# Kernel optimization log

Hardware: AMD Instinct MI355X
Metric: run time of the kernel (lower is better)

Reference implementation:

```python
import jax, jax.numpy as jnp
import numpy as np

LEFT, RIGHT = 64, 64  # left_size, right_size; hidden = LEFT*RIGHT = 4096


def _cayley(raw):
    """torch nn.utils.parametrizations.orthogonal(..., orthogonal_map='cayley',
    use_trivialization=False): A = triu(raw, 1); X = A - A^T (skew-symmetric);
    Q = (I - X/2)^{-1} (I + X/2)."""
    n = raw.shape[0]
    A = jnp.triu(raw, 1)
    X = A - A.T
    Id = jnp.eye(n, dtype=raw.dtype)
    return jnp.linalg.solve(Id - 0.5 * X, Id + 0.5 * X)


def setup_inputs() -> dict:
    key = jax.random.key(0)
    ks = jax.random.split(key, 8)
    B, S = 4, 2048
    H = LEFT * RIGHT
    inp = jax.random.normal(ks[0], (B, S, H), dtype=jnp.float32)
    raw_u_left = jax.random.normal(ks[1], (LEFT, LEFT), dtype=jnp.float32) * 0.02
    raw_v_left = jax.random.normal(ks[2], (LEFT, LEFT), dtype=jnp.float32) * 0.02
    raw_u_right = jax.random.normal(ks[3], (RIGHT, RIGHT), dtype=jnp.float32) * 0.02
    raw_v_right = jax.random.normal(ks[4], (RIGHT, RIGHT), dtype=jnp.float32) * 0.02
    diag_left = jnp.ones((LEFT,), dtype=jnp.float32)
    diag_right = jnp.ones((RIGHT,), dtype=jnp.float32)
    diag_scale = jnp.ones((H,), dtype=jnp.float32) + 0.01 * jax.random.normal(ks[5], (H,), dtype=jnp.float32)
    return {
        "inp": inp,
        "raw_u_left": raw_u_left,
        "raw_v_left": raw_v_left,
        "diag_left": diag_left,
        "raw_u_right": raw_u_right,
        "raw_v_right": raw_v_right,
        "diag_right": diag_right,
        "diag_scale": diag_scale,
        "inv_t": 0,
    }


def reference(inp, raw_u_left, raw_v_left, diag_left, raw_u_right, raw_v_right,
              diag_right, diag_scale, inv_t):
    # add_diag=True, use_diag=True path
    if inv_t:
        x = inp / diag_scale
        dl = 1.0 / diag_left
        dr = 1.0 / diag_right
    else:
        x = inp * diag_scale
        dl = diag_left
        dr = diag_right
    # Cayley-parametrized orthogonal factors
    Ul = _cayley(raw_u_left)
    Vl = _cayley(raw_v_left)
    Ur = _cayley(raw_u_right)
    Vr = _cayley(raw_v_right)
    # SVD-style reconstruction: M = U @ diag(d) @ V^T
    ML = (Ul * dl[None, :]) @ Vl.T  # [LEFT, LEFT]
    MR = (Ur * dr[None, :]) @ Vr.T  # [RIGHT, RIGHT]
    # Kronecker matmul: view last dim as [LEFT, RIGHT], out = ML^T @ X @ MR
    orig_shape = x.shape
    xb = x.reshape(-1, LEFT, RIGHT)  # [B*S, LEFT, RIGHT]
    out = jnp.einsum('bij,ik,jl->bkl', xb, ML, MR)
    return out.reshape(orig_shape)
```

## Files before the change

### kernel.cpp

```cpp
#include <hip/hip_runtime.h>
#include <hip/hip_bf16.h>

typedef short short8 __attribute__((ext_vector_type(8)));
typedef short short4v __attribute__((ext_vector_type(4)));
typedef float f32x4 __attribute__((ext_vector_type(4)));

#define HID 4096
#define CST 68

__device__ __forceinline__ unsigned short f2bf(float f) {
    unsigned int u = __float_as_uint(f);
    u = (u + 0x7FFFu + ((u >> 16) & 1u)) >> 16;
    return (unsigned short)u;
}

__device__ __forceinline__ f32x4 mm4(const float* SA, const float* SB, int i, int j0) {
    f32x4 acc = {0.f, 0.f, 0.f, 0.f};
#pragma unroll 8
    for (int k = 0; k < 64; ++k) {
        float a = SA[i * CST + k];
        acc += a * *reinterpret_cast<const f32x4*>(SB + k * CST + j0);
    }
    return acc;
}

__global__ __launch_bounds__(1024) void cayley_build_kernel(
    const float* __restrict__ rul, const float* __restrict__ rvl, const float* __restrict__ dl,
    const float* __restrict__ rur, const float* __restrict__ rvr, const float* __restrict__ dr,
    const int* __restrict__ invt,
    unsigned short* __restrict__ plb, unsigned short* __restrict__ mrtb)
{
    __shared__ __align__(16) float Yw[64 * CST], Aw[64 * CST], Pw[64 * CST];
    __shared__ __align__(16) float Qw[64 * CST], QTw[64 * CST];
    __shared__ float dd[64];

    const float* ru; const float* rv; const float* dv; unsigned short* ob;
    if (blockIdx.x == 0) { ru = rul; rv = rvl; dv = dl; ob = plb; }
    else                 { ru = rur; rv = rvr; dv = dr; ob = mrtb; }

    const int tid = threadIdx.x;
    const int i = tid >> 4;
    const int j0 = (tid & 15) << 2;

    for (int pass = 0; pass < 2; ++pass) {
        const float* raw = (pass == 0) ? ru : rv;
#pragma unroll
        for (int q = 0; q < 4; ++q) {
            int j = j0 + q;
            float v = 0.f;
            if (j > i)      v =  raw[i * 64 + j];
            else if (j < i) v = -raw[j * 64 + i];
            Yw[i * CST + j] = 0.5f * v;
        }
        __syncthreads();
        f32x4 a = mm4(Yw, Yw, i, j0);
        __syncthreads();
        *reinterpret_cast<f32x4*>(Aw + i * CST + j0) = a;
        *reinterpret_cast<f32x4*>(Pw + i * CST + j0) =
            a + *reinterpret_cast<const f32x4*>(Yw + i * CST + j0);
        __syncthreads();
        a = mm4(Pw, Aw, i, j0);
        __syncthreads();
        *reinterpret_cast<f32x4*>(Pw + i * CST + j0) += a;
        __syncthreads();
        a = mm4(Aw, Aw, i, j0);
        __syncthreads();
        *reinterpret_cast<f32x4*>(Aw + i * CST + j0) = a;
        __syncthreads();
        a = mm4(Pw, Aw, i, j0);
        __syncthreads();
        f32x4 p = *reinterpret_cast<const f32x4*>(Pw + i * CST + j0) + a;
#pragma unroll
        for (int q = 0; q < 4; ++q) {
            int j = j0 + q;
            float qv = ((i == j) ? 1.f : 0.f) + 2.f * p[q];
            if (pass == 0) Qw[i * CST + j]  = qv;
            else           QTw[j * CST + i] = qv;
        }
        __syncthreads();
    }
    if (tid < 64) { float d = dv[tid]; dd[tid] = (invt[0] != 0) ? (1.0f / d) : d; }
    __syncthreads();

    f32x4 m = {0.f, 0.f, 0.f, 0.f};
#pragma unroll 8
    for (int j = 0; j < 64; ++j) {
        float aa = Qw[i * CST + j] * dd[j];
        m += aa * *reinterpret_cast<const f32x4*>(QTw + j * CST + j0);
    }
#pragma unroll
    for (int q = 0; q < 4; ++q)
        ob[(j0 + q) * 64 + i] = f2bf(m[q]);
}

__global__ __launch_bounds__(256) void kron_kernel(
    const float* __restrict__ inp, const float* __restrict__ ds,
    const unsigned short* __restrict__ plb, const unsigned short* __restrict__ mrtb,
    const int* __restrict__ invt, float* __restrict__ out, int ntok)
{
    __shared__ __align__(16) unsigned short zbuf[4][64 * 72];
    const int w = threadIdx.x >> 6;
    const int lane = threadIdx.x & 63;
    const int l15 = lane & 15;
    const int lg = lane >> 4;
    unsigned short* Zt = zbuf[w];
    const int rowoff = l15 * 64 + lg * 8;

    short8 bmr[2][4], bpl[2][4];
#pragma unroll
    for (int tc = 0; tc < 4; ++tc)
#pragma unroll
        for (int s = 0; s < 2; ++s) {
            bmr[s][tc] = *reinterpret_cast<const short8*>(
                mrtb + (tc * 16 + l15) * 64 + s * 32 + lg * 8);
            bpl[s][tc] = *reinterpret_cast<const short8*>(
                plb + (tc * 16 + l15) * 64 + s * 32 + lg * 8);
        }
    const bool inv = (invt[0] != 0);

    const int t0 = (blockIdx.x * 4 + w) * 2;
#pragma unroll
    for (int it = 0; it < 2; ++it) {
        const int t = t0 + it;
        if (t >= ntok) break;
        const float* xt = inp + (size_t)t * HID;

        f32x4 acc[4][4];
        {
            f32x4 z = {0.f, 0.f, 0.f, 0.f};
#pragma unroll
            for (int a = 0; a < 4; ++a)
#pragma unroll
                for (int b = 0; b < 4; ++b) acc[a][b] = z;
        }
#pragma unroll
        for (int tr = 0; tr < 4; ++tr) {
            short8 a1[2];
#pragma unroll
            for (int s = 0; s < 2; ++s) {
                f32x4 x0 = *reinterpret_cast<const f32x4*>(xt + tr * 1024 + rowoff + s * 32);
                f32x4 x1 = *reinterpret_cast<const f32x4*>(xt + tr * 1024 + rowoff + s * 32 + 4);
                f32x4 d0 = *reinterpret_cast<const f32x4*>(ds + tr * 1024 + rowoff + s * 32);
                f32x4 d1 = *reinterpret_cast<const f32x4*>(ds + tr * 1024 + rowoff + s * 32 + 4);
                if (inv) {
#pragma unroll
                    for (int e = 0; e < 4; ++e) { x0[e] /= d0[e]; x1[e] /= d1[e]; }
                } else {
                    x0 *= d0; x1 *= d1;
                }
                short8 f;
#pragma unroll
                for (int e = 0; e < 4; ++e) {
                    f[e]     = (short)f2bf(x0[e]);
                    f[e + 4] = (short)f2bf(x1[e]);
                }
                a1[s] = f;
            }
#pragma unroll
            for (int tc = 0; tc < 4; ++tc) {
                acc[tr][tc] = __builtin_amdgcn_mfma_f32_16x16x32_bf16(a1[0], bmr[0][tc], acc[tr][tc], 0, 0, 0);
                acc[tr][tc] = __builtin_amdgcn_mfma_f32_16x16x32_bf16(a1[1], bmr[1][tc], acc[tr][tc], 0, 0, 0);
            }
        }

#pragma unroll
        for (int tc = 0; tc < 4; ++tc)
#pragma unroll
            for (int tr = 0; tr < 4; ++tr) {
                short4v zz;
#pragma unroll
                for (int r = 0; r < 4; ++r) zz[r] = (short)f2bf(acc[tr][tc][r]);
                *reinterpret_cast<short4v*>(Zt + (tc * 16 + l15) * 72 + tr * 16 + lg * 4) = zz;
            }

#pragma unroll
        for (int trY = 0; trY < 4; ++trY) {
            short8 a0 = *reinterpret_cast<const short8*>(Zt + (trY * 16 + l15) * 72 + lg * 8);
            short8 a1 = *reinterpret_cast<const short8*>(Zt + (trY * 16 + l15) * 72 + 32 + lg * 8);
#pragma unroll
            for (int tcY = 0; tcY < 4; ++tcY) {
                f32x4 y = {0.f, 0.f, 0.f, 0.f};
                y = __builtin_amdgcn_mfma_f32_16x16x32_bf16(a0, bpl[0][tcY], y, 0, 0, 0);
                y = __builtin_amdgcn_mfma_f32_16x16x32_bf16(a1, bpl[1][tcY], y, 0, 0, 0);
                f32x4* dst = reinterpret_cast<f32x4*>(
                    out + (size_t)t * HID + (tcY * 16 + l15) * 64 + trY * 16 + lg * 4);
                __builtin_nontemporal_store(y, dst);
            }
        }
    }
}

extern "C" void kernel_launch(void* const* d_in, const int* in_sizes, int n_in,
                              void* d_out, int out_size, void* d_ws, size_t ws_size,
                              hipStream_t stream) {
    const float* inp = (const float*)d_in[0];
    const float* rul = (const float*)d_in[1];
    const float* rvl = (const float*)d_in[2];
    const float* dl  = (const float*)d_in[3];
    const float* rur = (const float*)d_in[4];
    const float* rvr = (const float*)d_in[5];
    const float* dr  = (const float*)d_in[6];
    const float* ds  = (const float*)d_in[7];
    const int*   invt = (const int*)d_in[8];
    float* out = (float*)d_out;

    unsigned short* plb  = (unsigned short*)d_ws;
    unsigned short* mrtb = plb + 4096;

    const int ntok = in_sizes[0] / HID;

    hipLaunchKernelGGL(cayley_build_kernel, dim3(2), dim3(1024), 0, stream,
                       rul, rvl, dl, rur, rvr, dr, invt, plb, mrtb);
    const int nblk = (ntok + 7) / 8;
    hipLaunchKernelGGL(kron_kernel, dim3(nblk), dim3(256), 0, stream,
                       inp, ds, plb, mrtb, invt, out, ntok);
}
```

Before: 88.81 us.

## Split each token across four waves with shared LDS and register double-buffered prefetch

The kron kernel now has all four waves of a block work together on one token, each wave owning a 16-row slice, where before each wave handled whole tokens alone. The intermediate goes through one shared LDS tile with block barriers. The diag_scale slice is loaded once per thread into registers, with the reciprocal taken once for the inverse path instead of dividing per element. The next token's input is prefetched into alternating register sets, and blocks walk 8 tokens in sequence under a launch-bounds occupancy hint. This aims to hide global load latency and cut LDS use and redundant ds loads, but adds two block barriers per token and drops the nontemporal store hint.

Measured after the change: 90.41 us. No clear change (+1.8%).

```diff
diff --git a/kernel.cpp b/kernel.cpp
--- a/kernel.cpp
+++ b/kernel.cpp
@@ -7,6 +7,7 @@
 
 #define HID 4096
 #define CST 68
+#define TPB 8
 
 __device__ __forceinline__ unsigned short f2bf(float f) {
     unsigned int u = __float_as_uint(f);
@@ -93,18 +94,75 @@
         ob[(j0 + q) * 64 + i] = f2bf(m[q]);
 }
 
-__global__ __launch_bounds__(256) void kron_kernel(
+#define PREFETCH(X, PTR) do { \
+    const float* _p = (PTR); \
+    X##0 = *reinterpret_cast<const f32x4*>(_p); \
+    X##1 = *reinterpret_cast<const f32x4*>(_p + 4); \
+    X##2 = *reinterpret_cast<const f32x4*>(_p + 32); \
+    X##3 = *reinterpret_cast<const f32x4*>(_p + 36); \
+} while (0)
+
+#define TOKEN_BODY(T, X) do { \
+    short8 a1[2]; \
+    { \
+        f32x4 v00 = X##0 * dsr[0]; \
+        f32x4 v01 = X##1 * dsr[1]; \
+        f32x4 v10 = X##2 * dsr[2]; \
+        f32x4 v11 = X##3 * dsr[3]; \
+        short8 f0, f1; \
+        _Pragma("unroll") \
+        for (int e = 0; e < 4; ++e) { \
+            f0[e] = (short)f2bf(v00[e]); f0[e + 4] = (short)f2bf(v01[e]); \
+            f1[e] = (short)f2bf(v10[e]); f1[e + 4] = (short)f2bf(v11[e]); \
+        } \
+        a1[0] = f0; a1[1] = f1; \
+    } \
+    f32x4 acc[4]; \
+    { f32x4 z = {0.f,0.f,0.f,0.f}; acc[0]=z; acc[1]=z; acc[2]=z; acc[3]=z; } \
+    _Pragma("unroll") \
+    for (int s = 0; s < 2; ++s) { \
+        _Pragma("unroll") \
+        for (int tc = 0; tc < 4; ++tc) \
+            acc[tc] = __builtin_amdgcn_mfma_f32_16x16x32_bf16(a1[s], bmr[s][tc], acc[tc], 0, 0, 0); \
+    } \
+    _Pragma("unroll") \
+    for (int tc = 0; tc < 4; ++tc) { \
+        short4v zz; \
+        _Pragma("unroll") \
+        for (int r = 0; r < 4; ++r) zz[r] = (short)f2bf(acc[tc][r]); \
+        *reinterpret_cast<short4v*>(Zt + (tc * 16 + l15) * 72 + w * 16 + lg * 4) = zz; \
+    } \
+    asm volatile("s_waitcnt lgkmcnt(0)" ::: "memory"); \
+    __builtin_amdgcn_sched_barrier(0); \
+    __builtin_amdgcn_s_barrier(); \
+    short8 a20 = *reinterpret_cast<const short8*>(Zt + (w * 16 + l15) * 72 + lg * 8); \
+    short8 a21 = *reinterpret_cast<const short8*>(Zt + (w * 16 + l15) * 72 + 32 + lg * 8); \
+    f32x4 y[4]; \
+    { f32x4 z = {0.f,0.f,0.f,0.f}; y[0]=z; y[1]=z; y[2]=z; y[3]=z; } \
+    _Pragma("unroll") \
+    for (int tc = 0; tc < 4; ++tc) { \
+        y[tc] = __builtin_amdgcn_mfma_f32_16x16x32_bf16(a20, bpl[0][tc], y[tc], 0, 0, 0); \
+        y[tc] = __builtin_amdgcn_mfma_f32_16x16x32_bf16(a21, bpl[1][tc], y[tc], 0, 0, 0); \
+    } \
+    float* _op = out + (size_t)(T) * HID + w * 16 + lg * 4; \
+    _Pragma("unroll") \
+    for (int tc = 0; tc < 4; ++tc) \
+        *reinterpret_cast<f32x4*>(_op + (tc * 16 + l15) * 64) = y[tc]; \
+    __builtin_amdgcn_sched_barrier(0); \
+    __builtin_amdgcn_s_barrier(); \
+} while (0)
+
+__global__ __launch_bounds__(256, 3) void kron_kernel(
     const float* __restrict__ inp, const float* __restrict__ ds,
     const unsigned short* __restrict__ plb, const unsigned short* __restrict__ mrtb,
     const int* __restrict__ invt, float* __restrict__ out, int ntok)
 {
-    __shared__ __align__(16) unsigned short zbuf[4][64 * 72];
+    __shared__ __align__(16) unsigned short Zt[64 * 72];
     const int w = threadIdx.x >> 6;
     const int lane = threadIdx.x & 63;
     const int l15 = lane & 15;
     const int lg = lane >> 4;
-    unsigned short* Zt = zbuf[w];
-    const int rowoff = l15 * 64 + lg * 8;
+    const int rowbase = (w * 16 + l15) * 64 + lg * 8;
 
     short8 bmr[2][4], bpl[2][4];
 #pragma unroll
@@ -116,76 +174,36 @@
             bpl[s][tc] = *reinterpret_cast<const short8*>(
                 plb + (tc * 16 + l15) * 64 + s * 32 + lg * 8);
         }
+
     const bool inv = (invt[0] != 0);
-
-    const int t0 = (blockIdx.x * 4 + w) * 2;
-#pragma unroll
-    for (int it = 0; it < 2; ++it) {
+    f32x4 dsr[4];
+    dsr[0] = *reinterpret_cast<const f32x4*>(ds + rowbase);
+    dsr[1] = *reinterpret_cast<const f32x4*>(ds + rowbase + 4);
+    dsr[2] = *reinterpret_cast<const f32x4*>(ds + rowbase + 32);
+    dsr[3] = *reinterpret_cast<const f32x4*>(ds + rowbase + 36);
+    if (inv) {
+#pragma unroll
+        for (int q = 0; q < 4; ++q)
+#pragma unroll
+            for (int e = 0; e < 4; ++e) dsr[q][e] = 1.0f / dsr[q][e];
+    }
+
+    const int t0 = blockIdx.x * TPB;
+    int ntl = ntok - t0;
+    if (ntl <= 0) return;
+    if (ntl > TPB) ntl = TPB;
+
+    f32x4 xA0, xA1, xA2, xA3, xB0, xB1, xB2, xB3;
+    PREFETCH(xA, inp + (size_t)t0 * HID + rowbase);
+
+    for (int it = 0; it < ntl; ++it) {
         const int t = t0 + it;
-        if (t >= ntok) break;
-        const float* xt = inp + (size_t)t * HID;
-
-        f32x4 acc[4][4];
-        {
-            f32x4 z = {0.f, 0.f, 0.f, 0.f};
-#pragma unroll
-            for (int a = 0; a < 4; ++a)
-#pragma unroll
-                for (int b = 0; b < 4; ++b) acc[a][b] = z;
-        }
-#pragma unroll
-        for (int tr = 0; tr < 4; ++tr) {
-            short8 a1[2];
-#pragma unroll
-            for (int s = 0; s < 2; ++s) {
-                f32x4 x0 = *reinterpret_cast<const f32x4*>(xt + tr * 1024 + rowoff + s * 32);
-                f32x4 x1 = *reinterpret_cast<const f32x4*>(xt + tr * 1024 + rowoff + s * 32 + 4);
-                f32x4 d0 = *reinterpret_cast<const f32x4*>(ds + tr * 1024 + rowoff + s * 32);
-                f32x4 d1 = *reinterpret_cast<const f32x4*>(ds + tr * 1024 + rowoff + s * 32 + 4);
-                if (inv) {
-#pragma unroll
-                    for (int e = 0; e < 4; ++e) { x0[e] /= d0[e]; x1[e] /= d1[e]; }
-                } else {
-                    x0 *= d0; x1 *= d1;
-                }
-                short8 f;
-#pragma unroll
-                for (int e = 0; e < 4; ++e) {
-                    f[e]     = (short)f2bf(x0[e]);
-                    f[e + 4] = (short)f2bf(x1[e]);
-                }
-                a1[s] = f;
-            }
-#pragma unroll
-            for (int tc = 0; tc < 4; ++tc) {
-                acc[tr][tc] = __builtin_amdgcn_mfma_f32_16x16x32_bf16(a1[0], bmr[0][tc], acc[tr][tc], 0, 0, 0);
-                acc[tr][tc] = __builtin_amdgcn_mfma_f32_16x16x32_bf16(a1[1], bmr[1][tc], acc[tr][tc], 0, 0, 0);
-            }
-        }
-
-#pragma unroll
-        for (int tc = 0; tc < 4; ++tc)
-#pragma unroll
-            for (int tr = 0; tr < 4; ++tr) {
-                short4v zz;
-#pragma unroll
-                for (int r = 0; r < 4; ++r) zz[r] = (short)f2bf(acc[tr][tc][r]);
-                *reinterpret_cast<short4v*>(Zt + (tc * 16 + l15) * 72 + tr * 16 + lg * 4) = zz;
-            }
-
-#pragma unroll
-        for (int trY = 0; trY < 4; ++trY) {
-            short8 a0 = *reinterpret_cast<const short8*>(Zt + (trY * 16 + l15) * 72 + lg * 8);
-            short8 a1 = *reinterpret_cast<const short8*>(Zt + (trY * 16 + l15) * 72 + 32 + lg * 8);
-#pragma unroll
-            for (int tcY = 0; tcY < 4; ++tcY) {
-                f32x4 y = {0.f, 0.f, 0.f, 0.f};
-                y = __builtin_amdgcn_mfma_f32_16x16x32_bf16(a0, bpl[0][tcY], y, 0, 0, 0);
-                y = __builtin_amdgcn_mfma_f32_16x16x32_bf16(a1, bpl[1][tcY], y, 0, 0, 0);
-                f32x4* dst = reinterpret_cast<f32x4*>(
-                    out + (size_t)t * HID + (tcY * 16 + l15) * 64 + trY * 16 + lg * 4);
-                __builtin_nontemporal_store(y, dst);
-            }
+        if ((it & 1) == 0) {
+            if (it + 1 < ntl) PREFETCH(xB, inp + (size_t)(t + 1) * HID + rowbase);
+            TOKEN_BODY(t, xA);
+        } else {
+            if (it + 1 < ntl) PREFETCH(xA, inp + (size_t)(t + 1) * HID + rowbase);
+            TOKEN_BODY(t, xB);
         }
     }
 }
@@ -211,7 +229,7 @@
 
     hipLaunchKernelGGL(cayley_build_kernel, dim3(2), dim3(1024), 0, stream,
                        rul, rvl, dl, rur, rvr, dr, invt, plb, mrtb);
-    const int nblk = (ntok + 7) / 8;
+    const int nblk = (ntok + TPB - 1) / TPB;
     hipLaunchKernelGGL(kron_kernel, dim3(nblk), dim3(256), 0, stream,
                        inp, ds, plb, mrtb, invt, out, ntok);
 }
```

## Split tokens across warps by row band and software-pipeline input loads

Applied to the files above, without the earlier changes.

Reorganizes the Kronecker kernel so the four warps in a block share each token: each warp owns a 16-row band and exchanges intermediates through shared memory with block barriers. Each block now processes 16 tokens in groups of 4, and the next group's input loads are prefetched into registers while the current group is being computed. diag_scale is loaded once per thread and inverted up front, replacing the per-element division, and output stores become regular stores instead of nontemporal ones. The aim is to hide global load latency and cut redundant diag loads, at the cost of block-level barriers, higher register pressure and fewer blocks.

After: 87.68 us. No clear change (-1.3%).

```diff
diff --git a/kernel.cpp b/kernel.cpp
--- a/kernel.cpp
+++ b/kernel.cpp
@@ -7,6 +7,8 @@
 
 #define HID 4096
 #define CST 68
+#define G    4
+#define NGRP 4
 
 __device__ __forceinline__ unsigned short f2bf(float f) {
     unsigned int u = __float_as_uint(f);
@@ -93,18 +95,17 @@
         ob[(j0 + q) * 64 + i] = f2bf(m[q]);
 }
 
-__global__ __launch_bounds__(256) void kron_kernel(
+__global__ __launch_bounds__(256, 2) void kron_kernel(
     const float* __restrict__ inp, const float* __restrict__ ds,
     const unsigned short* __restrict__ plb, const unsigned short* __restrict__ mrtb,
     const int* __restrict__ invt, float* __restrict__ out, int ntok)
 {
-    __shared__ __align__(16) unsigned short zbuf[4][64 * 72];
+    __shared__ __align__(16) unsigned short Zt[G][64 * 72];
     const int w = threadIdx.x >> 6;
     const int lane = threadIdx.x & 63;
     const int l15 = lane & 15;
     const int lg = lane >> 4;
-    unsigned short* Zt = zbuf[w];
-    const int rowoff = l15 * 64 + lg * 8;
+    const int rowbase = (w * 16 + l15) * 64 + lg * 8;
 
     short8 bmr[2][4], bpl[2][4];
 #pragma unroll
@@ -116,77 +117,114 @@
             bpl[s][tc] = *reinterpret_cast<const short8*>(
                 plb + (tc * 16 + l15) * 64 + s * 32 + lg * 8);
         }
+
     const bool inv = (invt[0] != 0);
-
-    const int t0 = (blockIdx.x * 4 + w) * 2;
-#pragma unroll
-    for (int it = 0; it < 2; ++it) {
-        const int t = t0 + it;
-        if (t >= ntok) break;
-        const float* xt = inp + (size_t)t * HID;
-
-        f32x4 acc[4][4];
-        {
-            f32x4 z = {0.f, 0.f, 0.f, 0.f};
-#pragma unroll
-            for (int a = 0; a < 4; ++a)
-#pragma unroll
-                for (int b = 0; b < 4; ++b) acc[a][b] = z;
-        }
-#pragma unroll
-        for (int tr = 0; tr < 4; ++tr) {
-            short8 a1[2];
-#pragma unroll
-            for (int s = 0; s < 2; ++s) {
-                f32x4 x0 = *reinterpret_cast<const f32x4*>(xt + tr * 1024 + rowoff + s * 32);
-                f32x4 x1 = *reinterpret_cast<const f32x4*>(xt + tr * 1024 + rowoff + s * 32 + 4);
-                f32x4 d0 = *reinterpret_cast<const f32x4*>(ds + tr * 1024 + rowoff + s * 32);
-                f32x4 d1 = *reinterpret_cast<const f32x4*>(ds + tr * 1024 + rowoff + s * 32 + 4);
-                if (inv) {
-#pragma unroll
-                    for (int e = 0; e < 4; ++e) { x0[e] /= d0[e]; x1[e] /= d1[e]; }
-                } else {
-                    x0 *= d0; x1 *= d1;
+    f32x4 dsr[4];
+    dsr[0] = *reinterpret_cast<const f32x4*>(ds + rowbase);
+    dsr[1] = *reinterpret_cast<const f32x4*>(ds + rowbase + 4);
+    dsr[2] = *reinterpret_cast<const f32x4*>(ds + rowbase + 32);
+    dsr[3] = *reinterpret_cast<const f32x4*>(ds + rowbase + 36);
+    if (inv) {
+#pragma unroll
+        for (int q = 0; q < 4; ++q)
+#pragma unroll
+            for (int e = 0; e < 4; ++e) dsr[q][e] = 1.0f / dsr[q][e];
+    }
+
+    const int t00 = blockIdx.x * (G * NGRP);
+    if (t00 >= ntok) return;
+
+    f32x4 xb[G][4];
+
+    {
+        const float* p = inp + (size_t)t00 * HID + rowbase;
+#pragma unroll
+        for (int u = 0; u < G; ++u) {
+            if (t00 + u < ntok) {
+                const float* q = p + u * HID;
+                xb[u][0] = *reinterpret_cast<const f32x4*>(q);
+                xb[u][1] = *reinterpret_cast<const f32x4*>(q + 4);
+                xb[u][2] = *reinterpret_cast<const f32x4*>(q + 32);
+                xb[u][3] = *reinterpret_cast<const f32x4*>(q + 36);
+            }
+        }
+    }
+
+    for (int gg = 0; gg < NGRP; ++gg) {
+        const int tb = t00 + gg * G;
+
+        short8 a1[G][2];
+#pragma unroll
+        for (int u = 0; u < G; ++u) {
+            f32x4 v0 = xb[u][0] * dsr[0];
+            f32x4 v1 = xb[u][1] * dsr[1];
+            f32x4 v2 = xb[u][2] * dsr[2];
+            f32x4 v3 = xb[u][3] * dsr[3];
+            short8 f0, f1;
+#pragma unroll
+            for (int e = 0; e < 4; ++e) {
+                f0[e] = (short)f2bf(v0[e]); f0[e + 4] = (short)f2bf(v1[e]);
+                f1[e] = (short)f2bf(v2[e]); f1[e + 4] = (short)f2bf(v3[e]);
+            }
+            a1[u][0] = f0; a1[u][1] = f1;
+        }
+
+        if (gg + 1 < NGRP) {
+            const int tn = tb + G;
+            const float* p = inp + (size_t)tn * HID + rowbase;
+#pragma unroll
+            for (int u = 0; u < G; ++u) {
+                if (tn + u < ntok) {
+                    const float* q = p + u * HID;
+                    xb[u][0] = *reinterpret_cast<const f32x4*>(q);
+                    xb[u][1] = *reinterpret_cast<const f32x4*>(q + 4);
+                    xb[u][2] = *reinterpret_cast<const f32x4*>(q + 32);
+                    xb[u][3] = *reinterpret_cast<const f32x4*>(q + 36);
                 }
-                short8 f;
-#pragma unroll
-                for (int e = 0; e < 4; ++e) {
-                    f[e]     = (short)f2bf(x0[e]);
-                    f[e + 4] = (short)f2bf(x1[e]);
-                }
-                a1[s] = f;
-            }
+            }
+        }
+
+#pragma unroll
+        for (int u = 0; u < G; ++u) {
+            f32x4 acc[4];
+            { f32x4 z = {0.f,0.f,0.f,0.f}; acc[0]=z; acc[1]=z; acc[2]=z; acc[3]=z; }
+#pragma unroll
+            for (int s = 0; s < 2; ++s)
+#pragma unroll
+                for (int tc = 0; tc < 4; ++tc)
+                    acc[tc] = __builtin_amdgcn_mfma_f32_16x16x32_bf16(a1[u][s], bmr[s][tc], acc[tc], 0, 0, 0);
 #pragma unroll
             for (int tc = 0; tc < 4; ++tc) {
-                acc[tr][tc] = __builtin_amdgcn_mfma_f32_16x16x32_bf16(a1[0], bmr[0][tc], acc[tr][tc], 0, 0, 0);
-                acc[tr][tc] = __builtin_amdgcn_mfma_f32_16x16x32_bf16(a1[1], bmr[1][tc], acc[tr][tc], 0, 0, 0);
-            }
-        }
-
-#pragma unroll
-        for (int tc = 0; tc < 4; ++tc)
-#pragma unroll
-            for (int tr = 0; tr < 4; ++tr) {
                 short4v zz;
 #pragma unroll
-                for (int r = 0; r < 4; ++r) zz[r] = (short)f2bf(acc[tr][tc][r]);
-                *reinterpret_cast<short4v*>(Zt + (tc * 16 + l15) * 72 + tr * 16 + lg * 4) = zz;
-            }
-
-#pragma unroll
-        for (int trY = 0; trY < 4; ++trY) {
-            short8 a0 = *reinterpret_cast<const short8*>(Zt + (trY * 16 + l15) * 72 + lg * 8);
-            short8 a1 = *reinterpret_cast<const short8*>(Zt + (trY * 16 + l15) * 72 + 32 + lg * 8);
-#pragma unroll
-            for (int tcY = 0; tcY < 4; ++tcY) {
-                f32x4 y = {0.f, 0.f, 0.f, 0.f};
-                y = __builtin_amdgcn_mfma_f32_16x16x32_bf16(a0, bpl[0][tcY], y, 0, 0, 0);
-                y = __builtin_amdgcn_mfma_f32_16x16x32_bf16(a1, bpl[1][tcY], y, 0, 0, 0);
-                f32x4* dst = reinterpret_cast<f32x4*>(
-                    out + (size_t)t * HID + (tcY * 16 + l15) * 64 + trY * 16 + lg * 4);
-                __builtin_nontemporal_store(y, dst);
-            }
-        }
+                for (int r = 0; r < 4; ++r) zz[r] = (short)f2bf(acc[tc][r]);
+                *reinterpret_cast<short4v*>(&Zt[u][(tc * 16 + l15) * 72 + w * 16 + lg * 4]) = zz;
+            }
+        }
+        asm volatile("s_waitcnt lgkmcnt(0)" ::: "memory");
+        __builtin_amdgcn_sched_barrier(0);
+        __builtin_amdgcn_s_barrier();
+
+#pragma unroll
+        for (int u = 0; u < G; ++u) {
+            short8 a20 = *reinterpret_cast<const short8*>(&Zt[u][(w * 16 + l15) * 72 + lg * 8]);
+            short8 a21 = *reinterpret_cast<const short8*>(&Zt[u][(w * 16 + l15) * 72 + 32 + lg * 8]);
+            f32x4 y[4];
+            { f32x4 z = {0.f,0.f,0.f,0.f}; y[0]=z; y[1]=z; y[2]=z; y[3]=z; }
+#pragma unroll
+            for (int tc = 0; tc < 4; ++tc) {
+                y[tc] = __builtin_amdgcn_mfma_f32_16x16x32_bf16(a20, bpl[0][tc], y[tc], 0, 0, 0);
+                y[tc] = __builtin_amdgcn_mfma_f32_16x16x32_bf16(a21, bpl[1][tc], y[tc], 0, 0, 0);
+            }
+            if (tb + u < ntok) {
+                float* op = out + (size_t)(tb + u) * HID + w * 16 + lg * 4;
+#pragma unroll
+                for (int tc = 0; tc < 4; ++tc)
+                    *reinterpret_cast<f32x4*>(op + (tc * 16 + l15) * 64) = y[tc];
+            }
+        }
+        __builtin_amdgcn_sched_barrier(0);
+        __builtin_amdgcn_s_barrier();
     }
 }
 
@@ -211,7 +249,8 @@
 
     hipLaunchKernelGGL(cayley_build_kernel, dim3(2), dim3(1024), 0, stream,
                        rul, rvl, dl, rur, rvr, dr, invt, plb, mrtb);
-    const int nblk = (ntok + 7) / 8;
+    const int tpb = G * NGRP;
+    const int nblk = (ntok + tpb - 1) / tpb;
     hipLaunchKernelGGL(kron_kernel, dim3(nblk), dim3(256), 0, stream,
                        inp, ds, plb, mrtb, invt, out, ntok);
 }
```

## Restructure kron kernel with 32x32 MFMA, swizzled LDS staging, one token per wave

Applied to the files above, without the earlier changes.

The Kronecker matmul kernel is rewritten so each wave handles one token. Input is loaded fully coalesced into XOR-swizzled LDS, then both stages run on 32x32x16 bf16 MFMA instead of 16x16x32, with the intermediate kept in swizzled LDS. The grid doubles and launch bounds request four blocks per CU to raise occupancy. Output stores become scalar, 32-lane-contiguous writes instead of 16-byte nontemporal stores, which may cost store efficiency on this bandwidth-bound kernel.

After: 87.84 us. Within noise of the previous version (-1.1%).

```diff
diff --git a/kernel.cpp b/kernel.cpp
--- a/kernel.cpp
+++ b/kernel.cpp
@@ -4,6 +4,7 @@
 typedef short short8 __attribute__((ext_vector_type(8)));
 typedef short short4v __attribute__((ext_vector_type(4)));
 typedef float f32x4 __attribute__((ext_vector_type(4)));
+typedef float f32x16 __attribute__((ext_vector_type(16)));
 
 #define HID 4096
 #define CST 68
@@ -93,101 +94,119 @@
         ob[(j0 + q) * 64 + i] = f2bf(m[q]);
 }
 
-__global__ __launch_bounds__(256) void kron_kernel(
+__global__ __launch_bounds__(256, 4) void kron_kernel(
     const float* __restrict__ inp, const float* __restrict__ ds,
     const unsigned short* __restrict__ plb, const unsigned short* __restrict__ mrtb,
     const int* __restrict__ invt, float* __restrict__ out, int ntok)
 {
-    __shared__ __align__(16) unsigned short zbuf[4][64 * 72];
+    __shared__ __align__(16) unsigned char sbuf[4][8192];
     const int w = threadIdx.x >> 6;
     const int lane = threadIdx.x & 63;
-    const int l15 = lane & 15;
-    const int lg = lane >> 4;
-    unsigned short* Zt = zbuf[w];
-    const int rowoff = l15 * 64 + lg * 8;
-
-    short8 bmr[2][4], bpl[2][4];
-#pragma unroll
-    for (int tc = 0; tc < 4; ++tc)
-#pragma unroll
-        for (int s = 0; s < 2; ++s) {
-            bmr[s][tc] = *reinterpret_cast<const short8*>(
-                mrtb + (tc * 16 + l15) * 64 + s * 32 + lg * 8);
-            bpl[s][tc] = *reinterpret_cast<const short8*>(
-                plb + (tc * 16 + l15) * 64 + s * 32 + lg * 8);
-        }
+    const int r = lane & 31;
+    const int h = lane >> 5;
+    unsigned char* S = sbuf[w];
+
+    const int t = blockIdx.x * 4 + w;
+    if (t >= ntok) return;
     const bool inv = (invt[0] != 0);
 
-    const int t0 = (blockIdx.x * 4 + w) * 2;
-#pragma unroll
-    for (int it = 0; it < 2; ++it) {
-        const int t = t0 + it;
-        if (t >= ntok) break;
-        const float* xt = inp + (size_t)t * HID;
-
-        f32x4 acc[4][4];
-        {
-            f32x4 z = {0.f, 0.f, 0.f, 0.f};
-#pragma unroll
-            for (int a = 0; a < 4; ++a)
-#pragma unroll
-                for (int b = 0; b < 4; ++b) acc[a][b] = z;
-        }
-#pragma unroll
-        for (int tr = 0; tr < 4; ++tr) {
-            short8 a1[2];
-#pragma unroll
-            for (int s = 0; s < 2; ++s) {
-                f32x4 x0 = *reinterpret_cast<const f32x4*>(xt + tr * 1024 + rowoff + s * 32);
-                f32x4 x1 = *reinterpret_cast<const f32x4*>(xt + tr * 1024 + rowoff + s * 32 + 4);
-                f32x4 d0 = *reinterpret_cast<const f32x4*>(ds + tr * 1024 + rowoff + s * 32);
-                f32x4 d1 = *reinterpret_cast<const f32x4*>(ds + tr * 1024 + rowoff + s * 32 + 4);
-                if (inv) {
-#pragma unroll
-                    for (int e = 0; e < 4; ++e) { x0[e] /= d0[e]; x1[e] /= d1[e]; }
-                } else {
-                    x0 *= d0; x1 *= d1;
-                }
-                short8 f;
-#pragma unroll
-                for (int e = 0; e < 4; ++e) {
-                    f[e]     = (short)f2bf(x0[e]);
-                    f[e + 4] = (short)f2bf(x1[e]);
-                }
-                a1[s] = f;
+    const float* xt = inp + (size_t)t * HID;
+    const int c = lane & 7;
+    const int mr0 = lane >> 3;
+#pragma unroll
+    for (int s = 0; s < 8; ++s) {
+        const int fi = s * 512 + lane * 8;
+        f32x4 x0 = *reinterpret_cast<const f32x4*>(xt + fi);
+        f32x4 x1 = *reinterpret_cast<const f32x4*>(xt + fi + 4);
+        f32x4 d0 = *reinterpret_cast<const f32x4*>(ds + fi);
+        f32x4 d1 = *reinterpret_cast<const f32x4*>(ds + fi + 4);
+        if (inv) {
+#pragma unroll
+            for (int e = 0; e < 4; ++e) { x0[e] /= d0[e]; x1[e] /= d1[e]; }
+        } else {
+            x0 *= d0; x1 *= d1;
+        }
+        short8 f;
+#pragma unroll
+        for (int e = 0; e < 4; ++e) {
+            f[e]     = (short)f2bf(x0[e]);
+            f[e + 4] = (short)f2bf(x1[e]);
+        }
+        const int m = s * 8 + mr0;
+        *reinterpret_cast<short8*>(S + ((m * 8 + (c ^ (m & 7))) << 4)) = f;
+    }
+    asm volatile("s_waitcnt lgkmcnt(0)" ::: "memory");
+    __builtin_amdgcn_sched_barrier(0);
+
+    short8 a1[2][4];
+#pragma unroll
+    for (int mt = 0; mt < 2; ++mt)
+#pragma unroll
+        for (int kt = 0; kt < 4; ++kt)
+            a1[mt][kt] = *reinterpret_cast<const short8*>(
+                S + (((32 * mt + r) * 8 + ((2 * kt + h) ^ (r & 7))) << 4));
+    short8 b1[4][2];
+#pragma unroll
+    for (int kt = 0; kt < 4; ++kt)
+#pragma unroll
+        for (int nt = 0; nt < 2; ++nt)
+            b1[kt][nt] = *reinterpret_cast<const short8*>(
+                (const short*)mrtb + (32 * nt + r) * 64 + 16 * kt + 8 * h);
+
+    asm volatile("s_waitcnt lgkmcnt(0)" ::: "memory");
+    __builtin_amdgcn_sched_barrier(0);
+
+#pragma unroll
+    for (int mt = 0; mt < 2; ++mt)
+#pragma unroll
+        for (int nt = 0; nt < 2; ++nt) {
+            f32x16 acc = {0.f};
+#pragma unroll
+            for (int kt = 0; kt < 4; ++kt)
+                acc = __builtin_amdgcn_mfma_f32_32x32x16_bf16(a1[mt][kt], b1[kt][nt], acc, 0, 0, 0);
+            const int l = 32 * nt + r;
+#pragma unroll
+            for (int q = 0; q < 4; ++q) {
+                short4v zz;
+#pragma unroll
+                for (int e = 0; e < 4; ++e) zz[e] = (short)f2bf(acc[4 * q + e]);
+                *reinterpret_cast<short4v*>(
+                    S + (((l * 8 + ((4 * mt + q) ^ (l & 7))) << 4) + 8 * h)) = zz;
             }
-#pragma unroll
-            for (int tc = 0; tc < 4; ++tc) {
-                acc[tr][tc] = __builtin_amdgcn_mfma_f32_16x16x32_bf16(a1[0], bmr[0][tc], acc[tr][tc], 0, 0, 0);
-                acc[tr][tc] = __builtin_amdgcn_mfma_f32_16x16x32_bf16(a1[1], bmr[1][tc], acc[tr][tc], 0, 0, 0);
+        }
+    asm volatile("s_waitcnt lgkmcnt(0)" ::: "memory");
+    __builtin_amdgcn_sched_barrier(0);
+
+    short8 b2[4][2];
+#pragma unroll
+    for (int kt = 0; kt < 4; ++kt)
+#pragma unroll
+        for (int nt = 0; nt < 2; ++nt)
+            b2[kt][nt] = *reinterpret_cast<const short8*>(
+                S + (((32 * nt + r) * 8 + ((2 * kt + h) ^ (r & 7))) << 4));
+    short8 a2[2][4];
+#pragma unroll
+    for (int mt = 0; mt < 2; ++mt)
+#pragma unroll
+        for (int kt = 0; kt < 4; ++kt)
+            a2[mt][kt] = *reinterpret_cast<const short8*>(
+                (const short*)plb + (32 * mt + r) * 64 + 16 * kt + 8 * h);
+
+    float* op = out + (size_t)t * HID;
+#pragma unroll
+    for (int mt = 0; mt < 2; ++mt)
+#pragma unroll
+        for (int nt = 0; nt < 2; ++nt) {
+            f32x16 acc = {0.f};
+#pragma unroll
+            for (int kt = 0; kt < 4; ++kt)
+                acc = __builtin_amdgcn_mfma_f32_32x32x16_bf16(a2[mt][kt], b2[kt][nt], acc, 0, 0, 0);
+#pragma unroll
+            for (int g = 0; g < 16; ++g) {
+                const int k = 32 * mt + (g & 3) + 8 * (g >> 2) + 4 * h;
+                op[k * 64 + 32 * nt + r] = acc[g];
             }
         }
-
-#pragma unroll
-        for (int tc = 0; tc < 4; ++tc)
-#pragma unroll
-            for (int tr = 0; tr < 4; ++tr) {
-                short4v zz;
-#pragma unroll
-                for (int r = 0; r < 4; ++r) zz[r] = (short)f2bf(acc[tr][tc][r]);
-                *reinterpret_cast<short4v*>(Zt + (tc * 16 + l15) * 72 + tr * 16 + lg * 4) = zz;
-            }
-
-#pragma unroll
-        for (int trY = 0; trY < 4; ++trY) {
-            short8 a0 = *reinterpret_cast<const short8*>(Zt + (trY * 16 + l15) * 72 + lg * 8);
-            short8 a1 = *reinterpret_cast<const short8*>(Zt + (trY * 16 + l15) * 72 + 32 + lg * 8);
-#pragma unroll
-            for (int tcY = 0; tcY < 4; ++tcY) {
-                f32x4 y = {0.f, 0.f, 0.f, 0.f};
-                y = __builtin_amdgcn_mfma_f32_16x16x32_bf16(a0, bpl[0][tcY], y, 0, 0, 0);
-                y = __builtin_amdgcn_mfma_f32_16x16x32_bf16(a1, bpl[1][tcY], y, 0, 0, 0);
-                f32x4* dst = reinterpret_cast<f32x4*>(
-                    out + (size_t)t * HID + (tcY * 16 + l15) * 64 + trY * 16 + lg * 4);
-                __builtin_nontemporal_store(y, dst);
-            }
-        }
-    }
 }
 
 extern "C" void kernel_launch(void* const* d_in, const int* in_sizes, int n_in,
@@ -211,7 +230,7 @@
 
     hipLaunchKernelGGL(cayley_build_kernel, dim3(2), dim3(1024), 0, stream,
                        rul, rvl, dl, rur, rvr, dr, invt, plb, mrtb);
-    const int nblk = (ntok + 7) / 8;
+    const int nblk = (ntok + 3) / 4;
     hipLaunchKernelGGL(kron_kernel, dim3(nblk), dim3(256), 0, stream,
                        inp, ds, plb, mrtb, invt, out, ntok);
 }
```
